# Kernel tuning notes

Hardware: AMD Instinct MI355X
Metric: run time of the kernel (lower is better)

Reference implementation:

```python
import jax, jax.numpy as jnp
import numpy as np


def setup_inputs() -> dict:
    key = jax.random.key(0)
    k_user, k_music, k_label, k_mem, k_w = jax.random.split(key, 5)
    B, H, N = 65536, 1024, 256  # batch, hidden (=2*hidden_size), memory slots
    user = jax.random.normal(k_user, (B, H), dtype=jnp.float32)
    music = jax.random.normal(k_music, (B, H), dtype=jnp.float32)
    memory = jax.random.normal(k_mem, (N, H), dtype=jnp.float32) * (1.0 / np.sqrt(H).astype(np.float32))
    W_out = jax.random.normal(k_w, (H, 2), dtype=jnp.float32) * (1.0 / np.sqrt(H).astype(np.float32))
    b_out = jnp.zeros((2,), dtype=jnp.float32)
    label = jax.random.randint(k_label, (B,), 0, 2, dtype=jnp.int64 if jax.config.jax_enable_x64 else jnp.int32)
    return {"user": user, "music": music, "memory": memory, "W_out": W_out, "b_out": b_out, "label": label}


def reference(user, music, memory, W_out, b_out, label):
    # s = user * music  (elementwise interaction)  [B, H]
    s = user * music
    # classification head: Linear(hidden, 2)
    out_result = s @ W_out + b_out  # [B, 2]
    # memory read: softmax(s @ memory^T) @ memory
    attn = jax.nn.softmax(s @ memory.T, axis=1)  # [B, N]
    rel = attn @ memory  # [B, H]
    # translational score: ||user + rel - music||_2 per row
    diff = user + rel - music
    score = jnp.sqrt(jnp.sum(diff * diff, axis=1))  # [B]
    mask = (2 * label - 1).astype(score.dtype)  # {-1, +1}
    loss = jnp.mean(mask * score)
    return loss, out_result
```

## Files before the change

kernel.cpp:

```cpp
#include <hip/hip_runtime.h>
#include <hip/hip_bf16.h>

typedef float ff4 __attribute__((ext_vector_type(4)));
typedef short s8v __attribute__((ext_vector_type(8)));
typedef unsigned int u4v __attribute__((ext_vector_type(4)));

#define Hd 1024
#define Nn 256
#define KC 32
#define NCHUNK 32
#define SPAD 36
#define APAD 264

__device__ __forceinline__ unsigned bf16r(float f) {
    unsigned u = __builtin_bit_cast(unsigned, f);
    return (u + 0x7FFFu + ((u >> 16) & 1u)) >> 16;
}

__device__ __forceinline__ void glds16(void* lds, const void* g) {
    __builtin_amdgcn_global_load_lds(
        (const __attribute__((address_space(1))) unsigned int*)g,
        (__attribute__((address_space(3))) unsigned int*)lds, 16, 0, 0);
}

__global__ void conv_mem_kernel(const float* __restrict__ mem, unsigned short* __restrict__ memB) {
    int g = blockIdx.x * 256 + threadIdx.x;
    int c = g >> 10;
    int r = (g >> 2) & 255;
    int col0 = (g & 3) * 8;
    const float* src = mem + (size_t)r * Hd + c * KC + col0;
    ff4 a = *(const ff4*)src;
    ff4 b = *(const ff4*)(src + 4);
    u4v v;
    v[0] = bf16r(a[0]) | (bf16r(a[1]) << 16);
    v[1] = bf16r(a[2]) | (bf16r(a[3]) << 16);
    v[2] = bf16r(b[0]) | (bf16r(b[1]) << 16);
    v[3] = bf16r(b[2]) | (bf16r(b[3]) << 16);
    *(u4v*)(memB + (size_t)g * 8) = v;
}

__global__ void conv_w_kernel(const float* __restrict__ Wout, unsigned short* __restrict__ Wbf) {
    int t = threadIdx.x;
    int c = t >> 7;
    int h0 = (t & 127) * 8;
    u4v v;
#pragma unroll
    for (int j = 0; j < 4; ++j) {
        unsigned lo = bf16r(Wout[(h0 + 2 * j) * 2 + c]);
        unsigned hi = bf16r(Wout[(h0 + 2 * j + 1) * 2 + c]);
        v[j] = lo | (hi << 16);
    }
    *(u4v*)(Wbf + (size_t)c * Hd + h0) = v;
}

__global__ __launch_bounds__(256) void gram_kernel(const float* __restrict__ mem,
                                                   unsigned short* __restrict__ Gbf) {
    __shared__ float LA[32][132];
    __shared__ float LB[32][132];
    const int t = threadIdx.x;
    const int bi = blockIdx.x >> 3, bj = blockIdx.x & 7;
    const int j = t & 31, i0 = t >> 5;
    float acc0 = 0.f, acc1 = 0.f, acc2 = 0.f, acc3 = 0.f;
    for (int kc = 0; kc < Hd; kc += 128) {
        __syncthreads();
#pragma unroll
        for (int q = 0; q < 4; ++q) {
            int c = t + q * 256;
            int r = c >> 5, fc = (c & 31) << 2;
            *(ff4*)&LA[r][fc] = *(const ff4*)(mem + (size_t)(bi * 32 + r) * Hd + kc + fc);
            *(ff4*)&LB[r][fc] = *(const ff4*)(mem + (size_t)(bj * 32 + r) * Hd + kc + fc);
        }
        __syncthreads();
#pragma unroll 4
        for (int kk = 0; kk < 128; kk += 4) {
            ff4 b = *(const ff4*)&LB[j][kk];
            ff4 a0 = *(const ff4*)&LA[i0][kk];
            ff4 a1 = *(const ff4*)&LA[i0 + 8][kk];
            ff4 a2 = *(const ff4*)&LA[i0 + 16][kk];
            ff4 a3 = *(const ff4*)&LA[i0 + 24][kk];
            acc0 += a0[0]*b[0] + a0[1]*b[1] + a0[2]*b[2] + a0[3]*b[3];
            acc1 += a1[0]*b[0] + a1[1]*b[1] + a1[2]*b[2] + a1[3]*b[3];
            acc2 += a2[0]*b[0] + a2[1]*b[1] + a2[2]*b[2] + a2[3]*b[3];
            acc3 += a3[0]*b[0] + a3[1]*b[1] + a3[2]*b[2] + a3[3]*b[3];
        }
    }
    const int gj = bj * 32 + j;
    Gbf[(size_t)(bi * 32 + i0 +  0) * Nn + gj] = (unsigned short)bf16r(acc0);
    Gbf[(size_t)(bi * 32 + i0 +  8) * Nn + gj] = (unsigned short)bf16r(acc1);
    Gbf[(size_t)(bi * 32 + i0 + 16) * Nn + gj] = (unsigned short)bf16r(acc2);
    Gbf[(size_t)(bi * 32 + i0 + 24) * Nn + gj] = (unsigned short)bf16r(acc3);
}

__global__ __launch_bounds__(256, 2) void fused_kernel(
    const float* __restrict__ user, const float* __restrict__ music,
    const float* __restrict__ bout, const int* __restrict__ label,
    const unsigned short* __restrict__ memB,
    const unsigned short* __restrict__ Wbf,
    const unsigned short* __restrict__ Gbf,
    float* __restrict__ out, float* __restrict__ partials)
{
    __shared__ __align__(16) unsigned char smem[51200];
    unsigned short* sM = (unsigned short*)smem;
    unsigned short* sS = (unsigned short*)(smem + 32768);
    unsigned short* sD = (unsigned short*)(smem + 41984);
    unsigned short* sAttn = (unsigned short*)smem;

    const int t = threadIdx.x;
    const int w = t >> 6;
    const int l = t & 63;
    const int la = l & 15, lb = l >> 4;
    const int row0 = blockIdx.x * 64;
    const int sr = t >> 2, kp = t & 3;

    const float* uR = user  + (size_t)(row0 + sr) * Hd + kp * 8;
    const float* mR = music + (size_t)(row0 + sr) * Hd + kp * 8;
    const char* gsrc = (const char*)memB + w * 4096 + l * 16;

    ff4 accL[16], accD[16];
#pragma unroll
    for (int i = 0; i < 16; ++i) { accL[i] = (ff4)0.0f; accD[i] = (ff4)0.0f; }
    ff4 accH = (ff4)0.0f;
    float sd2 = 0.f;

#pragma unroll
    for (int i = 0; i < 4; ++i)
        glds16(smem + w * 4096 + i * 1024, gsrc + i * 1024);
    {
        ff4 ua = *(const ff4*)(uR), ub = *(const ff4*)(uR + 4);
        ff4 ma = *(const ff4*)(mR), mb = *(const ff4*)(mR + 4);
        u4v vs, vd;
#pragma unroll
        for (int j = 0; j < 2; ++j) {
            ff4 uu = j ? ub : ua, mm = j ? mb : ma;
            float s0 = uu[0]*mm[0], s1 = uu[1]*mm[1], s2 = uu[2]*mm[2], s3 = uu[3]*mm[3];
            float d0 = uu[0]-mm[0], d1 = uu[1]-mm[1], d2 = uu[2]-mm[2], d3 = uu[3]-mm[3];
            sd2 = fmaf(d0,d0,sd2); sd2 = fmaf(d1,d1,sd2); sd2 = fmaf(d2,d2,sd2); sd2 = fmaf(d3,d3,sd2);
            vs[2*j]   = bf16r(s0) | (bf16r(s1) << 16);
            vs[2*j+1] = bf16r(s2) | (bf16r(s3) << 16);
            vd[2*j]   = bf16r(d0) | (bf16r(d1) << 16);
            vd[2*j+1] = bf16r(d2) | (bf16r(d3) << 16);
        }
        *(u4v*)(sS + sr * SPAD + kp * 8) = vs;
        *(u4v*)(sD + sr * SPAD + kp * 8) = vd;
    }
    __syncthreads();

    for (int c = 0; c < NCHUNK; ++c) {
        const int cur = c & 1;
        s8v bW = *(const s8v*)(Wbf + (size_t)(la < 2 ? la : 1) * Hd + c * KC + lb * 8);
        ff4 pua, pub, pma, pmb;
        if (c + 1 < NCHUNK) {
#pragma unroll
            for (int i = 0; i < 4; ++i)
                glds16(smem + (cur ^ 1) * 16384 + w * 4096 + i * 1024,
                       gsrc + (size_t)(c + 1) * 16384 + i * 1024);
            pua = *(const ff4*)(uR + (c + 1) * KC);
            pub = *(const ff4*)(uR + (c + 1) * KC + 4);
            pma = *(const ff4*)(mR + (c + 1) * KC);
            pmb = *(const ff4*)(mR + (c + 1) * KC + 4);
        }
        s8v aS = *(const s8v*)(sS + cur * 2304 + (w * 16 + la) * SPAD + lb * 8);
        s8v aD = *(const s8v*)(sD + cur * 2304 + (w * 16 + la) * SPAD + lb * 8);
#pragma unroll
        for (int nt = 0; nt < 16; ++nt) {
            s8v bM = *(const s8v*)(sM + cur * 8192 + (nt * 16 + la) * 32 + lb * 8);
            accL[nt] = __builtin_amdgcn_mfma_f32_16x16x32_bf16(aS, bM, accL[nt], 0, 0, 0);
            accD[nt] = __builtin_amdgcn_mfma_f32_16x16x32_bf16(aD, bM, accD[nt], 0, 0, 0);
        }
        accH = __builtin_amdgcn_mfma_f32_16x16x32_bf16(aS, bW, accH, 0, 0, 0);
        if (c + 1 < NCHUNK) {
            u4v vs, vd;
#pragma unroll
            for (int j = 0; j < 2; ++j) {
                ff4 uu = j ? pub : pua, mm = j ? pmb : pma;
                float s0 = uu[0]*mm[0], s1 = uu[1]*mm[1], s2 = uu[2]*mm[2], s3 = uu[3]*mm[3];
                float d0 = uu[0]-mm[0], d1 = uu[1]-mm[1], d2 = uu[2]-mm[2], d3 = uu[3]-mm[3];
                sd2 = fmaf(d0,d0,sd2); sd2 = fmaf(d1,d1,sd2); sd2 = fmaf(d2,d2,sd2); sd2 = fmaf(d3,d3,sd2);
                vs[2*j]   = bf16r(s0) | (bf16r(s1) << 16);
                vs[2*j+1] = bf16r(s2) | (bf16r(s3) << 16);
                vd[2*j]   = bf16r(d0) | (bf16r(d1) << 16);
                vd[2*j+1] = bf16r(d2) | (bf16r(d3) << 16);
            }
            *(u4v*)(sS + (cur ^ 1) * 2304 + sr * SPAD + kp * 8) = vs;
            *(u4v*)(sD + (cur ^ 1) * 2304 + sr * SPAD + kp * 8) = vd;
        }
        __syncthreads();
    }

    if (la < 2) {
#pragma unroll
        for (int j = 0; j < 4; ++j) {
            int gr = row0 + w * 16 + lb * 4 + j;
            out[1 + gr * 2 + la] = accH[j] + bout[la];
        }
    }
    sd2 += __shfl_xor(sd2, 1);
    sd2 += __shfl_xor(sd2, 2);

    float mr0, mr1, mr2, mr3;
    {
        ff4 mx = accL[0];
#pragma unroll
        for (int nt = 1; nt < 16; ++nt) {
            mx[0] = fmaxf(mx[0], accL[nt][0]); mx[1] = fmaxf(mx[1], accL[nt][1]);
            mx[2] = fmaxf(mx[2], accL[nt][2]); mx[3] = fmaxf(mx[3], accL[nt][3]);
        }
#pragma unroll
        for (int s = 1; s < 16; s <<= 1) {
            mx[0] = fmaxf(mx[0], __shfl_xor(mx[0], s));
            mx[1] = fmaxf(mx[1], __shfl_xor(mx[1], s));
            mx[2] = fmaxf(mx[2], __shfl_xor(mx[2], s));
            mx[3] = fmaxf(mx[3], __shfl_xor(mx[3], s));
        }
        mr0 = mx[0]; mr1 = mx[1]; mr2 = mx[2]; mr3 = mx[3];
    }
    ff4 sumv = (ff4)0.0f;
#pragma unroll
    for (int nt = 0; nt < 16; ++nt) {
        accL[nt][0] = __expf(accL[nt][0] - mr0);
        accL[nt][1] = __expf(accL[nt][1] - mr1);
        accL[nt][2] = __expf(accL[nt][2] - mr2);
        accL[nt][3] = __expf(accL[nt][3] - mr3);
        sumv[0] += accL[nt][0]; sumv[1] += accL[nt][1];
        sumv[2] += accL[nt][2]; sumv[3] += accL[nt][3];
    }
#pragma unroll
    for (int s = 1; s < 16; s <<= 1) {
        sumv[0] += __shfl_xor(sumv[0], s); sumv[1] += __shfl_xor(sumv[1], s);
        sumv[2] += __shfl_xor(sumv[2], s); sumv[3] += __shfl_xor(sumv[3], s);
    }
    const float i0v = 1.0f / sumv[0], i1v = 1.0f / sumv[1];
    const float i2v = 1.0f / sumv[2], i3v = 1.0f / sumv[3];
    ff4 cross = (ff4)0.0f;
#pragma unroll
    for (int nt = 0; nt < 16; ++nt) {
        accL[nt][0] *= i0v; accL[nt][1] *= i1v; accL[nt][2] *= i2v; accL[nt][3] *= i3v;
        cross[0] = fmaf(accL[nt][0], accD[nt][0], cross[0]);
        cross[1] = fmaf(accL[nt][1], accD[nt][1], cross[1]);
        cross[2] = fmaf(accL[nt][2], accD[nt][2], cross[2]);
        cross[3] = fmaf(accL[nt][3], accD[nt][3], cross[3]);
    }
#pragma unroll
    for (int s = 1; s < 16; s <<= 1) {
        cross[0] += __shfl_xor(cross[0], s); cross[1] += __shfl_xor(cross[1], s);
        cross[2] += __shfl_xor(cross[2], s); cross[3] += __shfl_xor(cross[3], s);
    }

    unsigned short* myAttn = sAttn + w * (16 * APAD);
    {
        const int rb = lb << 2;
#pragma unroll
        for (int nt = 0; nt < 16; ++nt) {
            const int cc = nt * 16 + la;
            myAttn[(rb + 0) * APAD + cc] = (unsigned short)bf16r(accL[nt][0]);
            myAttn[(rb + 1) * APAD + cc] = (unsigned short)bf16r(accL[nt][1]);
            myAttn[(rb + 2) * APAD + cc] = (unsigned short)bf16r(accL[nt][2]);
            myAttn[(rb + 3) * APAD + cc] = (unsigned short)bf16r(accL[nt][3]);
        }
    }

    ff4 accG[16];
#pragma unroll
    for (int i = 0; i < 16; ++i) accG[i] = (ff4)0.0f;
#pragma unroll
    for (int ks = 0; ks < 8; ++ks) {
        const int ko = ks * 32 + (lb << 3);
        s8v aA = *(const s8v*)(myAttn + la * APAD + ko);
#pragma unroll
        for (int nt = 0; nt < 16; ++nt) {
            s8v bG = *(const s8v*)(Gbf + (size_t)(nt * 16 + la) * Nn + ko);
            accG[nt] = __builtin_amdgcn_mfma_f32_16x16x32_bf16(aA, bG, accG[nt], 0, 0, 0);
        }
    }
    ff4 quad = (ff4)0.0f;
#pragma unroll
    for (int nt = 0; nt < 16; ++nt) {
        quad[0] = fmaf(accL[nt][0], accG[nt][0], quad[0]);
        quad[1] = fmaf(accL[nt][1], accG[nt][1], quad[1]);
        quad[2] = fmaf(accL[nt][2], accG[nt][2], quad[2]);
        quad[3] = fmaf(accL[nt][3], accG[nt][3], quad[3]);
    }
#pragma unroll
    for (int s = 1; s < 16; s <<= 1) {
        quad[0] += __shfl_xor(quad[0], s); quad[1] += __shfl_xor(quad[1], s);
        quad[2] += __shfl_xor(quad[2], s); quad[3] += __shfl_xor(quad[3], s);
    }

    float sdr = __shfl(sd2, (((lb << 2) + la) << 2) & 63);
    float val = 0.f;
    if (la < 4) {
        const int r = lb * 4 + la;
        float cr = (la == 0) ? cross[0] : (la == 1) ? cross[1] : (la == 2) ? cross[2] : cross[3];
        float qd = (la == 0) ? quad[0]  : (la == 1) ? quad[1]  : (la == 2) ? quad[2]  : quad[3];
        float s2 = sdr + 2.0f * cr + qd;
        float sc = sqrtf(fmaxf(s2, 0.0f));
        const int gr = row0 + w * 16 + r;
        val = (float)(2 * label[gr] - 1) * sc;
    }
#pragma unroll
    for (int s = 1; s < 64; s <<= 1) val += __shfl_xor(val, s);
    if (l == 0) partials[blockIdx.x * 4 + w] = val;
}

__global__ void finalize_kernel(const float* __restrict__ partials, float* __restrict__ out,
                                int np, float invB) {
    const int t = threadIdx.x;
    float v = 0.f;
    for (int i = t; i < np; i += 256) v += partials[i];
#pragma unroll
    for (int s = 1; s < 64; s <<= 1) v += __shfl_xor(v, s);
    __shared__ float ws4[4];
    if ((t & 63) == 0) ws4[t >> 6] = v;
    __syncthreads();
    if (t == 0) out[0] = (ws4[0] + ws4[1] + ws4[2] + ws4[3]) * invB;
}

extern "C" void kernel_launch(void* const* d_in, const int* in_sizes, int n_in,
                              void* d_out, int out_size, void* d_ws, size_t ws_size,
                              hipStream_t stream) {
    const float* user  = (const float*)d_in[0];
    const float* music = (const float*)d_in[1];
    const float* mem   = (const float*)d_in[2];
    const float* Wout  = (const float*)d_in[3];
    const float* bout  = (const float*)d_in[4];
    const int*   label = (const int*)d_in[5];
    const int Bn   = in_sizes[0] / Hd;
    const int nblk = Bn / 64;

    unsigned short* memB = (unsigned short*)d_ws;
    unsigned short* Wbf  = (unsigned short*)((char*)d_ws + 524288);
    unsigned short* Gbf  = (unsigned short*)((char*)d_ws + 524288 + 4096);
    float* partials      = (float*)((char*)d_ws + 524288 + 4096 + 131072);

    conv_mem_kernel<<<128, 256, 0, stream>>>(mem, memB);
    conv_w_kernel<<<1, 256, 0, stream>>>(Wout, Wbf);
    gram_kernel<<<64, 256, 0, stream>>>(mem, Gbf);
    fused_kernel<<<nblk, 256, 0, stream>>>(user, music, bout, label, memB, Wbf, Gbf,
                                           (float*)d_out, partials);
    finalize_kernel<<<1, 256, 0, stream>>>(partials, (float*)d_out, nblk * 4, 1.0f / (float)Bn);
}
```

Before: 255.6 us.

## Load user/music A-fragments directly into registers, widen K chunk, swizzle memory tiles

Each lane now loads its own user/music row slices straight from global memory and forms the bf16 product and difference fragments in registers. This drops the LDS staging of s/d and one barrier's worth of LDS traffic per chunk. The K chunk doubles to 64 (16 chunks), the memory tiles are stored with an XOR swizzle to avoid LDS bank conflicts, and the loop is unrolled twice with register double-buffered fragments and explicit waitcnt/barrier scheduling. LDS use grows to 64KB per block, which may limit occupancy, and the per-lane global loads are less coalesced.

```diff
diff --git a/kernel.cpp b/kernel.cpp
--- a/kernel.cpp
+++ b/kernel.cpp
@@ -4,12 +4,12 @@
 typedef float ff4 __attribute__((ext_vector_type(4)));
 typedef short s8v __attribute__((ext_vector_type(8)));
 typedef unsigned int u4v __attribute__((ext_vector_type(4)));
+typedef unsigned int u2v __attribute__((ext_vector_type(2)));
 
 #define Hd 1024
 #define Nn 256
-#define KC 32
-#define NCHUNK 32
-#define SPAD 36
+#define KC 64
+#define NCHUNK 16
 #define APAD 264
 
 __device__ __forceinline__ unsigned bf16r(float f) {
@@ -25,18 +25,19 @@
 
 __global__ void conv_mem_kernel(const float* __restrict__ mem, unsigned short* __restrict__ memB) {
     int g = blockIdx.x * 256 + threadIdx.x;
-    int c = g >> 10;
-    int r = (g >> 2) & 255;
-    int col0 = (g & 3) * 8;
-    const float* src = mem + (size_t)r * Hd + c * KC + col0;
-    ff4 a = *(const ff4*)src;
-    ff4 b = *(const ff4*)(src + 4);
+    int b = g & 7;
+    int r = (g >> 3) & 255;
+    int c = g >> 11;
+    const float* src = mem + (size_t)r * Hd + c * KC + b * 8;
+    ff4 a0 = *(const ff4*)src;
+    ff4 a1 = *(const ff4*)(src + 4);
     u4v v;
-    v[0] = bf16r(a[0]) | (bf16r(a[1]) << 16);
-    v[1] = bf16r(a[2]) | (bf16r(a[3]) << 16);
-    v[2] = bf16r(b[0]) | (bf16r(b[1]) << 16);
-    v[3] = bf16r(b[2]) | (bf16r(b[3]) << 16);
-    *(u4v*)(memB + (size_t)g * 8) = v;
+    v[0] = bf16r(a0[0]) | (bf16r(a0[1]) << 16);
+    v[1] = bf16r(a0[2]) | (bf16r(a0[3]) << 16);
+    v[2] = bf16r(a1[0]) | (bf16r(a1[1]) << 16);
+    v[3] = bf16r(a1[2]) | (bf16r(a1[3]) << 16);
+    size_t dst = (size_t)c * 32768 + (size_t)r * 128 + (size_t)((b ^ (r & 7)) * 16);
+    *(u4v*)((char*)memB + dst) = v;
 }
 
 __global__ void conv_w_kernel(const float* __restrict__ Wout, unsigned short* __restrict__ Wbf) {
@@ -91,6 +92,48 @@
     Gbf[(size_t)(bi * 32 + i0 + 24) * Nn + gj] = (unsigned short)bf16r(acc3);
 }
 
+struct Frags { s8v s0, s1, d0, d1; };
+struct UMr { ff4 ua, ub, uc, ud, ma, mb, mc, md; };
+
+__device__ __forceinline__ void load_um(UMr& r, const float* uR, const float* mR, int c) {
+    const float* up = uR + c * KC;
+    const float* mp = mR + c * KC;
+    r.ua = *(const ff4*)(up);      r.ub = *(const ff4*)(up + 4);
+    r.uc = *(const ff4*)(up + 32); r.ud = *(const ff4*)(up + 36);
+    r.ma = *(const ff4*)(mp);      r.mb = *(const ff4*)(mp + 4);
+    r.mc = *(const ff4*)(mp + 32); r.md = *(const ff4*)(mp + 36);
+}
+
+__device__ __forceinline__ void cvt_frag(const UMr& r, Frags& f, float& sd2) {
+    s8v as, ad;
+#pragma unroll
+    for (int q = 0; q < 4; ++q) {
+        float ss = r.ua[q]*r.ma[q], dd = r.ua[q]-r.ma[q];
+        sd2 = fmaf(dd, dd, sd2);
+        as[q] = (short)bf16r(ss); ad[q] = (short)bf16r(dd);
+    }
+#pragma unroll
+    for (int q = 0; q < 4; ++q) {
+        float ss = r.ub[q]*r.mb[q], dd = r.ub[q]-r.mb[q];
+        sd2 = fmaf(dd, dd, sd2);
+        as[4+q] = (short)bf16r(ss); ad[4+q] = (short)bf16r(dd);
+    }
+    f.s0 = as; f.d0 = ad;
+#pragma unroll
+    for (int q = 0; q < 4; ++q) {
+        float ss = r.uc[q]*r.mc[q], dd = r.uc[q]-r.mc[q];
+        sd2 = fmaf(dd, dd, sd2);
+        as[q] = (short)bf16r(ss); ad[q] = (short)bf16r(dd);
+    }
+#pragma unroll
+    for (int q = 0; q < 4; ++q) {
+        float ss = r.ud[q]*r.md[q], dd = r.ud[q]-r.md[q];
+        sd2 = fmaf(dd, dd, sd2);
+        as[4+q] = (short)bf16r(ss); ad[4+q] = (short)bf16r(dd);
+    }
+    f.s1 = as; f.d1 = ad;
+}
+
 __global__ __launch_bounds__(256, 2) void fused_kernel(
     const float* __restrict__ user, const float* __restrict__ music,
     const float* __restrict__ bout, const int* __restrict__ label,
@@ -99,10 +142,7 @@
     const unsigned short* __restrict__ Gbf,
     float* __restrict__ out, float* __restrict__ partials)
 {
-    __shared__ __align__(16) unsigned char smem[51200];
-    unsigned short* sM = (unsigned short*)smem;
-    unsigned short* sS = (unsigned short*)(smem + 32768);
-    unsigned short* sD = (unsigned short*)(smem + 41984);
+    __shared__ __align__(16) unsigned char smem[65536];
     unsigned short* sAttn = (unsigned short*)smem;
 
     const int t = threadIdx.x;
@@ -110,11 +150,15 @@
     const int l = t & 63;
     const int la = l & 15, lb = l >> 4;
     const int row0 = blockIdx.x * 64;
-    const int sr = t >> 2, kp = t & 3;
-
-    const float* uR = user  + (size_t)(row0 + sr) * Hd + kp * 8;
-    const float* mR = music + (size_t)(row0 + sr) * Hd + kp * 8;
-    const char* gsrc = (const char*)memB + w * 4096 + l * 16;
+    const int myrow = row0 + w * 16 + la;
+
+    const float* uR = user  + (size_t)myrow * Hd + lb * 8;
+    const float* mR = music + (size_t)myrow * Hd + lb * 8;
+    const char* gsrcW = (const char*)memB + w * 8192 + l * 16;
+    const unsigned short* wrowB = Wbf + (size_t)(la < 2 ? la : 1) * Hd + lb * 8;
+
+    const int off0 = la * 128 + ((lb) ^ (la & 7)) * 16;
+    const int off1 = la * 128 + ((4 + lb) ^ (la & 7)) * 16;
 
     ff4 accL[16], accD[16];
 #pragma unroll
@@ -122,70 +166,58 @@
     ff4 accH = (ff4)0.0f;
     float sd2 = 0.f;
 
-#pragma unroll
-    for (int i = 0; i < 4; ++i)
-        glds16(smem + w * 4096 + i * 1024, gsrc + i * 1024);
-    {
-        ff4 ua = *(const ff4*)(uR), ub = *(const ff4*)(uR + 4);
-        ff4 ma = *(const ff4*)(mR), mb = *(const ff4*)(mR + 4);
-        u4v vs, vd;
-#pragma unroll
-        for (int j = 0; j < 2; ++j) {
-            ff4 uu = j ? ub : ua, mm = j ? mb : ma;
-            float s0 = uu[0]*mm[0], s1 = uu[1]*mm[1], s2 = uu[2]*mm[2], s3 = uu[3]*mm[3];
-            float d0 = uu[0]-mm[0], d1 = uu[1]-mm[1], d2 = uu[2]-mm[2], d3 = uu[3]-mm[3];
-            sd2 = fmaf(d0,d0,sd2); sd2 = fmaf(d1,d1,sd2); sd2 = fmaf(d2,d2,sd2); sd2 = fmaf(d3,d3,sd2);
-            vs[2*j]   = bf16r(s0) | (bf16r(s1) << 16);
-            vs[2*j+1] = bf16r(s2) | (bf16r(s3) << 16);
-            vd[2*j]   = bf16r(d0) | (bf16r(d1) << 16);
-            vd[2*j+1] = bf16r(d2) | (bf16r(d3) << 16);
-        }
-        *(u4v*)(sS + sr * SPAD + kp * 8) = vs;
-        *(u4v*)(sD + sr * SPAD + kp * 8) = vd;
-    }
-    __syncthreads();
-
-    for (int c = 0; c < NCHUNK; ++c) {
-        const int cur = c & 1;
-        s8v bW = *(const s8v*)(Wbf + (size_t)(la < 2 ? la : 1) * Hd + c * KC + lb * 8);
-        ff4 pua, pub, pma, pmb;
-        if (c + 1 < NCHUNK) {
-#pragma unroll
-            for (int i = 0; i < 4; ++i)
-                glds16(smem + (cur ^ 1) * 16384 + w * 4096 + i * 1024,
-                       gsrc + (size_t)(c + 1) * 16384 + i * 1024);
-            pua = *(const ff4*)(uR + (c + 1) * KC);
-            pub = *(const ff4*)(uR + (c + 1) * KC + 4);
-            pma = *(const ff4*)(mR + (c + 1) * KC);
-            pmb = *(const ff4*)(mR + (c + 1) * KC + 4);
-        }
-        s8v aS = *(const s8v*)(sS + cur * 2304 + (w * 16 + la) * SPAD + lb * 8);
-        s8v aD = *(const s8v*)(sD + cur * 2304 + (w * 16 + la) * SPAD + lb * 8);
-#pragma unroll
-        for (int nt = 0; nt < 16; ++nt) {
-            s8v bM = *(const s8v*)(sM + cur * 8192 + (nt * 16 + la) * 32 + lb * 8);
-            accL[nt] = __builtin_amdgcn_mfma_f32_16x16x32_bf16(aS, bM, accL[nt], 0, 0, 0);
-            accD[nt] = __builtin_amdgcn_mfma_f32_16x16x32_bf16(aD, bM, accD[nt], 0, 0, 0);
-        }
-        accH = __builtin_amdgcn_mfma_f32_16x16x32_bf16(aS, bW, accH, 0, 0, 0);
-        if (c + 1 < NCHUNK) {
-            u4v vs, vd;
-#pragma unroll
-            for (int j = 0; j < 2; ++j) {
-                ff4 uu = j ? pub : pua, mm = j ? pmb : pma;
-                float s0 = uu[0]*mm[0], s1 = uu[1]*mm[1], s2 = uu[2]*mm[2], s3 = uu[3]*mm[3];
-                float d0 = uu[0]-mm[0], d1 = uu[1]-mm[1], d2 = uu[2]-mm[2], d3 = uu[3]-mm[3];
-                sd2 = fmaf(d0,d0,sd2); sd2 = fmaf(d1,d1,sd2); sd2 = fmaf(d2,d2,sd2); sd2 = fmaf(d3,d3,sd2);
-                vs[2*j]   = bf16r(s0) | (bf16r(s1) << 16);
-                vs[2*j+1] = bf16r(s2) | (bf16r(s3) << 16);
-                vd[2*j]   = bf16r(d0) | (bf16r(d1) << 16);
-                vd[2*j+1] = bf16r(d2) | (bf16r(d3) << 16);
-            }
-            *(u4v*)(sS + (cur ^ 1) * 2304 + sr * SPAD + kp * 8) = vs;
-            *(u4v*)(sD + (cur ^ 1) * 2304 + sr * SPAD + kp * 8) = vd;
-        }
-        __syncthreads();
-    }
+    Frags fA, fB;
+    UMr um;
+
+#pragma unroll
+    for (int i = 0; i < 8; ++i)
+        glds16(smem + w * 8192 + i * 1024, gsrcW + i * 1024);
+    __builtin_amdgcn_sched_barrier(0);
+    load_um(um, uR, mR, 0);
+    cvt_frag(um, fA, sd2);
+    __builtin_amdgcn_sched_barrier(0);
+    asm volatile("s_waitcnt vmcnt(0)" ::: "memory");
+    __builtin_amdgcn_s_barrier();
+    __builtin_amdgcn_sched_barrier(0);
+
+#define CHUNK_BODY(C, FC, FN, PF)                                               \
+    {                                                                           \
+        const int bsel = (C) & 1;                                               \
+        if (PF) {                                                               \
+            const char* gs = gsrcW + (size_t)((C) + 1) * 32768;                 \
+            _Pragma("unroll")                                                   \
+            for (int i = 0; i < 8; ++i)                                         \
+                glds16(smem + (bsel ^ 1) * 32768 + w * 8192 + i * 1024,         \
+                       gs + i * 1024);                                          \
+            __builtin_amdgcn_sched_barrier(0);                                  \
+        }                                                                       \
+        s8v bW0 = *(const s8v*)(wrowB + (C) * KC);                              \
+        s8v bW1 = *(const s8v*)(wrowB + (C) * KC + 32);                         \
+        if (PF) load_um(um, uR, mR, (C) + 1);                                   \
+        const unsigned char* mbase = smem + bsel * 32768;                       \
+        _Pragma("unroll")                                                       \
+        for (int nt = 0; nt < 16; ++nt) {                                       \
+            s8v bM0 = *(const s8v*)(mbase + nt * 2048 + off0);                  \
+            s8v bM1 = *(const s8v*)(mbase + nt * 2048 + off1);                  \
+            accL[nt] = __builtin_amdgcn_mfma_f32_16x16x32_bf16(FC.s0, bM0, accL[nt], 0, 0, 0); \
+            accD[nt] = __builtin_amdgcn_mfma_f32_16x16x32_bf16(FC.d0, bM0, accD[nt], 0, 0, 0); \
+            accL[nt] = __builtin_amdgcn_mfma_f32_16x16x32_bf16(FC.s1, bM1, accL[nt], 0, 0, 0); \
+            accD[nt] = __builtin_amdgcn_mfma_f32_16x16x32_bf16(FC.d1, bM1, accD[nt], 0, 0, 0); \
+        }                                                                       \
+        accH = __builtin_amdgcn_mfma_f32_16x16x32_bf16(FC.s0, bW0, accH, 0, 0, 0); \
+        accH = __builtin_amdgcn_mfma_f32_16x16x32_bf16(FC.s1, bW1, accH, 0, 0, 0); \
+        if (PF) cvt_frag(um, FN, sd2);                                          \
+        __builtin_amdgcn_sched_barrier(0);                                      \
+        asm volatile("s_waitcnt vmcnt(0)" ::: "memory");                        \
+        __builtin_amdgcn_s_barrier();                                           \
+        __builtin_amdgcn_sched_barrier(0);                                      \
+    }
+
+    for (int cc = 0; cc < NCHUNK; cc += 2) {
+        CHUNK_BODY(cc,     fA, fB, (cc     < NCHUNK - 1));
+        CHUNK_BODY(cc + 1, fB, fA, (cc + 1 < NCHUNK - 1));
+    }
+#undef CHUNK_BODY
 
     if (la < 2) {
 #pragma unroll
@@ -194,8 +226,8 @@
             out[1 + gr * 2 + la] = accH[j] + bout[la];
         }
     }
-    sd2 += __shfl_xor(sd2, 1);
-    sd2 += __shfl_xor(sd2, 2);
+    sd2 += __shfl_xor(sd2, 16);
+    sd2 += __shfl_xor(sd2, 32);
 
     float mr0, mr1, mr2, mr3;
     {
@@ -251,11 +283,11 @@
         const int rb = lb << 2;
 #pragma unroll
         for (int nt = 0; nt < 16; ++nt) {
-            const int cc = nt * 16 + la;
-            myAttn[(rb + 0) * APAD + cc] = (unsigned short)bf16r(accL[nt][0]);
-            myAttn[(rb + 1) * APAD + cc] = (unsigned short)bf16r(accL[nt][1]);
-            myAttn[(rb + 2) * APAD + cc] = (unsigned short)bf16r(accL[nt][2]);
-            myAttn[(rb + 3) * APAD + cc] = (unsigned short)bf16r(accL[nt][3]);
+            const int cc2 = nt * 16 + la;
+            myAttn[(rb + 0) * APAD + cc2] = (unsigned short)bf16r(accL[nt][0]);
+            myAttn[(rb + 1) * APAD + cc2] = (unsigned short)bf16r(accL[nt][1]);
+            myAttn[(rb + 2) * APAD + cc2] = (unsigned short)bf16r(accL[nt][2]);
+            myAttn[(rb + 3) * APAD + cc2] = (unsigned short)bf16r(accL[nt][3]);
         }
     }
 
@@ -286,10 +318,10 @@
         quad[2] += __shfl_xor(quad[2], s); quad[3] += __shfl_xor(quad[3], s);
     }
 
-    float sdr = __shfl(sd2, (((lb << 2) + la) << 2) & 63);
+    float sdr = __shfl(sd2, (lb << 2) + la);
     float val = 0.f;
     if (la < 4) {
-        const int r = lb * 4 + la;
+        const int r = (lb << 2) + la;
         float cr = (la == 0) ? cross[0] : (la == 1) ? cross[1] : (la == 2) ? cross[2] : cross[3];
         float qd = (la == 0) ? quad[0]  : (la == 1) ? quad[1]  : (la == 2) ? quad[2]  : quad[3];
         float s2 = sdr + 2.0f * cr + qd;
```

Measured after the change: 217.2 us. 1.18x faster.

## Load MFMA A-operands directly from global to registers, swizzle LDS, raise occupancy

Applied to the files above, without the earlier changes.

Each lane now loads its own user/music fragment straight into registers and forms the bf16 S and D operands in-register with packed convert instructions. This removes the LDS staging buffers for S and D and one sync per chunk. The memory tile is stored pre-swizzled by the conversion kernel, and the attention scratch uses an XOR swizzle in place of padding. Cutting LDS to 32KB allows three blocks per CU. Hand-placed waitcnt and barriers keep the global-to-LDS prefetch in flight, but the wraparound prefetch on the last chunk issues redundant loads, and the manual vmcnt counting is fragile.

```diff
diff --git a/kernel.cpp b/kernel.cpp
--- a/kernel.cpp
+++ b/kernel.cpp
@@ -9,12 +9,16 @@
 #define Nn 256
 #define KC 32
 #define NCHUNK 32
-#define SPAD 36
-#define APAD 264
 
 __device__ __forceinline__ unsigned bf16r(float f) {
     unsigned u = __builtin_bit_cast(unsigned, f);
     return (u + 0x7FFFu + ((u >> 16) & 1u)) >> 16;
+}
+
+__device__ __forceinline__ unsigned cvtpk(float lo, float hi) {
+    unsigned r;
+    asm("v_cvt_pk_bf16_f32 %0, %1, %2" : "=v"(r) : "v"(lo), "v"(hi));
+    return r;
 }
 
 __device__ __forceinline__ void glds16(void* lds, const void* g) {
@@ -25,18 +29,19 @@
 
 __global__ void conv_mem_kernel(const float* __restrict__ mem, unsigned short* __restrict__ memB) {
     int g = blockIdx.x * 256 + threadIdx.x;
+    int b = g & 3;
+    int r = (g >> 2) & 255;
     int c = g >> 10;
-    int r = (g >> 2) & 255;
-    int col0 = (g & 3) * 8;
-    const float* src = mem + (size_t)r * Hd + c * KC + col0;
-    ff4 a = *(const ff4*)src;
-    ff4 b = *(const ff4*)(src + 4);
+    const float* src = mem + (size_t)r * Hd + c * KC + b * 8;
+    ff4 a0 = *(const ff4*)src;
+    ff4 a1 = *(const ff4*)(src + 4);
     u4v v;
-    v[0] = bf16r(a[0]) | (bf16r(a[1]) << 16);
-    v[1] = bf16r(a[2]) | (bf16r(a[3]) << 16);
-    v[2] = bf16r(b[0]) | (bf16r(b[1]) << 16);
-    v[3] = bf16r(b[2]) | (bf16r(b[3]) << 16);
-    *(u4v*)(memB + (size_t)g * 8) = v;
+    v[0] = bf16r(a0[0]) | (bf16r(a0[1]) << 16);
+    v[1] = bf16r(a0[2]) | (bf16r(a0[3]) << 16);
+    v[2] = bf16r(a1[0]) | (bf16r(a1[1]) << 16);
+    v[3] = bf16r(a1[2]) | (bf16r(a1[3]) << 16);
+    size_t dst = (size_t)c * 16384 + (size_t)r * 64 + (size_t)((b ^ ((r >> 1) & 3)) * 16);
+    *(u4v*)((char*)memB + dst) = v;
 }
 
 __global__ void conv_w_kernel(const float* __restrict__ Wout, unsigned short* __restrict__ Wbf) {
@@ -91,7 +96,7 @@
     Gbf[(size_t)(bi * 32 + i0 + 24) * Nn + gj] = (unsigned short)bf16r(acc3);
 }
 
-__global__ __launch_bounds__(256, 2) void fused_kernel(
+__global__ __launch_bounds__(256, 3) void fused_kernel(
     const float* __restrict__ user, const float* __restrict__ music,
     const float* __restrict__ bout, const int* __restrict__ label,
     const unsigned short* __restrict__ memB,
@@ -99,10 +104,7 @@
     const unsigned short* __restrict__ Gbf,
     float* __restrict__ out, float* __restrict__ partials)
 {
-    __shared__ __align__(16) unsigned char smem[51200];
-    unsigned short* sM = (unsigned short*)smem;
-    unsigned short* sS = (unsigned short*)(smem + 32768);
-    unsigned short* sD = (unsigned short*)(smem + 41984);
+    __shared__ __align__(16) unsigned char smem[32768];
     unsigned short* sAttn = (unsigned short*)smem;
 
     const int t = threadIdx.x;
@@ -110,11 +112,13 @@
     const int l = t & 63;
     const int la = l & 15, lb = l >> 4;
     const int row0 = blockIdx.x * 64;
-    const int sr = t >> 2, kp = t & 3;
-
-    const float* uR = user  + (size_t)(row0 + sr) * Hd + kp * 8;
-    const float* mR = music + (size_t)(row0 + sr) * Hd + kp * 8;
-    const char* gsrc = (const char*)memB + w * 4096 + l * 16;
+    const int myrow = row0 + w * 16 + la;
+
+    const float* uR = user  + (size_t)myrow * Hd + lb * 8;
+    const float* mR = music + (size_t)myrow * Hd + lb * 8;
+    const char* gsrcW = (const char*)memB + w * 4096 + l * 16;
+    const unsigned short* wrowB = Wbf + (size_t)(la < 2 ? la : 1) * Hd + lb * 8;
+    const int myoff = la * 64 + ((lb ^ ((la >> 1) & 3)) << 4);
 
     ff4 accL[16], accD[16];
 #pragma unroll
@@ -124,68 +128,59 @@
 
 #pragma unroll
     for (int i = 0; i < 4; ++i)
-        glds16(smem + w * 4096 + i * 1024, gsrc + i * 1024);
-    {
-        ff4 ua = *(const ff4*)(uR), ub = *(const ff4*)(uR + 4);
-        ff4 ma = *(const ff4*)(mR), mb = *(const ff4*)(mR + 4);
-        u4v vs, vd;
-#pragma unroll
-        for (int j = 0; j < 2; ++j) {
-            ff4 uu = j ? ub : ua, mm = j ? mb : ma;
-            float s0 = uu[0]*mm[0], s1 = uu[1]*mm[1], s2 = uu[2]*mm[2], s3 = uu[3]*mm[3];
-            float d0 = uu[0]-mm[0], d1 = uu[1]-mm[1], d2 = uu[2]-mm[2], d3 = uu[3]-mm[3];
-            sd2 = fmaf(d0,d0,sd2); sd2 = fmaf(d1,d1,sd2); sd2 = fmaf(d2,d2,sd2); sd2 = fmaf(d3,d3,sd2);
-            vs[2*j]   = bf16r(s0) | (bf16r(s1) << 16);
-            vs[2*j+1] = bf16r(s2) | (bf16r(s3) << 16);
-            vd[2*j]   = bf16r(d0) | (bf16r(d1) << 16);
-            vd[2*j+1] = bf16r(d2) | (bf16r(d3) << 16);
-        }
-        *(u4v*)(sS + sr * SPAD + kp * 8) = vs;
-        *(u4v*)(sD + sr * SPAD + kp * 8) = vd;
-    }
-    __syncthreads();
+        glds16(smem + w * 4096 + i * 1024, gsrcW + i * 1024);
+    ff4 ua = *(const ff4*)(uR);
+    ff4 ub = *(const ff4*)(uR + 4);
+    ff4 ma = *(const ff4*)(mR);
+    ff4 mb = *(const ff4*)(mR + 4);
+    s8v bW = *(const s8v*)(wrowB);
+    __builtin_amdgcn_sched_barrier(0);
 
     for (int c = 0; c < NCHUNK; ++c) {
-        const int cur = c & 1;
-        s8v bW = *(const s8v*)(Wbf + (size_t)(la < 2 ? la : 1) * Hd + c * KC + lb * 8);
-        ff4 pua, pub, pma, pmb;
-        if (c + 1 < NCHUNK) {
-#pragma unroll
-            for (int i = 0; i < 4; ++i)
-                glds16(smem + (cur ^ 1) * 16384 + w * 4096 + i * 1024,
-                       gsrc + (size_t)(c + 1) * 16384 + i * 1024);
-            pua = *(const ff4*)(uR + (c + 1) * KC);
-            pub = *(const ff4*)(uR + (c + 1) * KC + 4);
-            pma = *(const ff4*)(mR + (c + 1) * KC);
-            pmb = *(const ff4*)(mR + (c + 1) * KC + 4);
-        }
-        s8v aS = *(const s8v*)(sS + cur * 2304 + (w * 16 + la) * SPAD + lb * 8);
-        s8v aD = *(const s8v*)(sD + cur * 2304 + (w * 16 + la) * SPAD + lb * 8);
+        const int bsel = c & 1;
+        asm volatile("s_waitcnt vmcnt(5)" ::: "memory");
+        __builtin_amdgcn_s_barrier();
+        __builtin_amdgcn_sched_barrier(0);
+
+        float s0 = ua[0]*ma[0], s1 = ua[1]*ma[1], s2 = ua[2]*ma[2], s3 = ua[3]*ma[3];
+        float s4 = ub[0]*mb[0], s5 = ub[1]*mb[1], s6 = ub[2]*mb[2], s7 = ub[3]*mb[3];
+        float d0 = ua[0]-ma[0], d1 = ua[1]-ma[1], d2 = ua[2]-ma[2], d3 = ua[3]-ma[3];
+        float d4 = ub[0]-mb[0], d5 = ub[1]-mb[1], d6 = ub[2]-mb[2], d7 = ub[3]-mb[3];
+        sd2 = fmaf(d0,d0,sd2); sd2 = fmaf(d1,d1,sd2); sd2 = fmaf(d2,d2,sd2); sd2 = fmaf(d3,d3,sd2);
+        sd2 = fmaf(d4,d4,sd2); sd2 = fmaf(d5,d5,sd2); sd2 = fmaf(d6,d6,sd2); sd2 = fmaf(d7,d7,sd2);
+        u4v ps, pd;
+        ps[0] = cvtpk(s0,s1); ps[1] = cvtpk(s2,s3); ps[2] = cvtpk(s4,s5); ps[3] = cvtpk(s6,s7);
+        pd[0] = cvtpk(d0,d1); pd[1] = cvtpk(d2,d3); pd[2] = cvtpk(d4,d5); pd[3] = cvtpk(d6,d7);
+        s8v fs = __builtin_bit_cast(s8v, ps);
+        s8v fd = __builtin_bit_cast(s8v, pd);
+
+        accH = __builtin_amdgcn_mfma_f32_16x16x32_bf16(fs, bW, accH, 0, 0, 0);
+
+        const int cn = (c + 1) & (NCHUNK - 1);
+#pragma unroll
+        for (int i = 0; i < 4; ++i)
+            glds16(smem + (bsel ^ 1) * 16384 + w * 4096 + i * 1024,
+                   gsrcW + (size_t)cn * 16384 + i * 1024);
+        ua = *(const ff4*)(uR + cn * KC);
+        ub = *(const ff4*)(uR + cn * KC + 4);
+        ma = *(const ff4*)(mR + cn * KC);
+        mb = *(const ff4*)(mR + cn * KC + 4);
+        bW = *(const s8v*)(wrowB + cn * KC);
+        __builtin_amdgcn_sched_barrier(0);
+
+        const unsigned char* mbase = smem + bsel * 16384;
 #pragma unroll
         for (int nt = 0; nt < 16; ++nt) {
-            s8v bM = *(const s8v*)(sM + cur * 8192 + (nt * 16 + la) * 32 + lb * 8);
-            accL[nt] = __builtin_amdgcn_mfma_f32_16x16x32_bf16(aS, bM, accL[nt], 0, 0, 0);
-            accD[nt] = __builtin_amdgcn_mfma_f32_16x16x32_bf16(aD, bM, accD[nt], 0, 0, 0);
-        }
-        accH = __builtin_amdgcn_mfma_f32_16x16x32_bf16(aS, bW, accH, 0, 0, 0);
-        if (c + 1 < NCHUNK) {
-            u4v vs, vd;
-#pragma unroll
-            for (int j = 0; j < 2; ++j) {
-                ff4 uu = j ? pub : pua, mm = j ? pmb : pma;
-                float s0 = uu[0]*mm[0], s1 = uu[1]*mm[1], s2 = uu[2]*mm[2], s3 = uu[3]*mm[3];
-                float d0 = uu[0]-mm[0], d1 = uu[1]-mm[1], d2 = uu[2]-mm[2], d3 = uu[3]-mm[3];
-                sd2 = fmaf(d0,d0,sd2); sd2 = fmaf(d1,d1,sd2); sd2 = fmaf(d2,d2,sd2); sd2 = fmaf(d3,d3,sd2);
-                vs[2*j]   = bf16r(s0) | (bf16r(s1) << 16);
-                vs[2*j+1] = bf16r(s2) | (bf16r(s3) << 16);
-                vd[2*j]   = bf16r(d0) | (bf16r(d1) << 16);
-                vd[2*j+1] = bf16r(d2) | (bf16r(d3) << 16);
-            }
-            *(u4v*)(sS + (cur ^ 1) * 2304 + sr * SPAD + kp * 8) = vs;
-            *(u4v*)(sD + (cur ^ 1) * 2304 + sr * SPAD + kp * 8) = vd;
-        }
-        __syncthreads();
-    }
+            s8v bM = *(const s8v*)(mbase + nt * 1024 + myoff);
+            accL[nt] = __builtin_amdgcn_mfma_f32_16x16x32_bf16(fs, bM, accL[nt], 0, 0, 0);
+            accD[nt] = __builtin_amdgcn_mfma_f32_16x16x32_bf16(fd, bM, accD[nt], 0, 0, 0);
+        }
+        __builtin_amdgcn_sched_barrier(0);
+    }
+
+    asm volatile("s_waitcnt vmcnt(0)" ::: "memory");
+    __builtin_amdgcn_s_barrier();
+    __builtin_amdgcn_sched_barrier(0);
 
     if (la < 2) {
 #pragma unroll
@@ -194,8 +189,8 @@
             out[1 + gr * 2 + la] = accH[j] + bout[la];
         }
     }
-    sd2 += __shfl_xor(sd2, 1);
-    sd2 += __shfl_xor(sd2, 2);
+    sd2 += __shfl_xor(sd2, 16);
+    sd2 += __shfl_xor(sd2, 32);
 
     float mr0, mr1, mr2, mr3;
     {
@@ -246,16 +241,17 @@
         cross[2] += __shfl_xor(cross[2], s); cross[3] += __shfl_xor(cross[3], s);
     }
 
-    unsigned short* myAttn = sAttn + w * (16 * APAD);
+    unsigned short* myAttn = sAttn + w * 4096;
     {
         const int rb = lb << 2;
+        const int cl = la & 7;
 #pragma unroll
         for (int nt = 0; nt < 16; ++nt) {
-            const int cc = nt * 16 + la;
-            myAttn[(rb + 0) * APAD + cc] = (unsigned short)bf16r(accL[nt][0]);
-            myAttn[(rb + 1) * APAD + cc] = (unsigned short)bf16r(accL[nt][1]);
-            myAttn[(rb + 2) * APAD + cc] = (unsigned short)bf16r(accL[nt][2]);
-            myAttn[(rb + 3) * APAD + cc] = (unsigned short)bf16r(accL[nt][3]);
+            const int nb = nt * 2 + (la >> 3);
+            myAttn[(rb + 0) * 256 + ((nb ^ ((rb + 0) & 7)) << 3) + cl] = (unsigned short)bf16r(accL[nt][0]);
+            myAttn[(rb + 1) * 256 + ((nb ^ ((rb + 1) & 7)) << 3) + cl] = (unsigned short)bf16r(accL[nt][1]);
+            myAttn[(rb + 2) * 256 + ((nb ^ ((rb + 2) & 7)) << 3) + cl] = (unsigned short)bf16r(accL[nt][2]);
+            myAttn[(rb + 3) * 256 + ((nb ^ ((rb + 3) & 7)) << 3) + cl] = (unsigned short)bf16r(accL[nt][3]);
         }
     }
 
@@ -265,7 +261,7 @@
 #pragma unroll
     for (int ks = 0; ks < 8; ++ks) {
         const int ko = ks * 32 + (lb << 3);
-        s8v aA = *(const s8v*)(myAttn + la * APAD + ko);
+        s8v aA = *(const s8v*)(myAttn + la * 256 + (((ks * 4 + lb) ^ (la & 7)) << 3));
 #pragma unroll
         for (int nt = 0; nt < 16; ++nt) {
             s8v bG = *(const s8v*)(Gbf + (size_t)(nt * 16 + la) * Nn + ko);
@@ -286,10 +282,10 @@
         quad[2] += __shfl_xor(quad[2], s); quad[3] += __shfl_xor(quad[3], s);
     }
 
-    float sdr = __shfl(sd2, (((lb << 2) + la) << 2) & 63);
+    float sdr = __shfl(sd2, (lb << 2) + la);
     float val = 0.f;
     if (la < 4) {
-        const int r = lb * 4 + la;
+        const int r = (lb << 2) + la;
         float cr = (la == 0) ? cross[0] : (la == 1) ? cross[1] : (la == 2) ? cross[2] : cross[3];
         float qd = (la == 0) ? quad[0]  : (la == 1) ? quad[1]  : (la == 2) ? quad[2]  : quad[3];
         float s2 = sdr + 2.0f * cr + qd;
```

Result: slower. 531.8 us (+108.1%).
